# Performance work log

Measured on AMD Instinct MI355X. Metric: run time of the kernel, lower is better.

The kernel has to match this reference:

```python
import jax, jax.numpy as jnp
import numpy as np

DROP_PROB = 0.1
BLOCK_SIZE = 7  # odd -> no even-size trim branch
N, C, H, W = 64, 256, 28, 28


def conv3x3(x, w):
    # x: [N,C,H,W], w: [O,I,3,3], stride 1, SAME padding
    return jax.lax.conv_general_dilated(
        x, w, window_strides=(1, 1), padding='SAME',
        dimension_numbers=('NCHW', 'OIHW', 'NCHW'))


def setup_inputs() -> dict:
    key = jax.random.key(0)
    k1, k2, k3, k4 = jax.random.split(key, 4)
    x = jax.random.normal(k1, (N, C, H, W), jnp.float32)
    # learned conv weights for the two branches (layer3 and premodel.layer3)
    w_layer3 = jax.random.normal(k2, (C, C, 3, 3), jnp.float32) * 0.05
    w_pre = jax.random.normal(k3, (C, C, 3, 3), jnp.float32) * 0.05
    # uniform draws used for the Bernoulli(gamma) drop mask, shape (N,H,W)
    mask_u = jax.random.uniform(k4, (N, H, W), jnp.float32)
    return {'x': x, 'w_layer3': w_layer3, 'w_pre': w_pre, 'mask_u': mask_u}


def reference(x, w_layer3, w_pre, mask_u):
    gamma = DROP_PROB / (BLOCK_SIZE ** 2)
    a = conv3x3(x, w_layer3)   # x = self.layer3(x)
    b = conv3x3(x, w_pre)      # output4 = self.premodel.layer3(x)
    # mask = (rand(N,H,W) < gamma).float()
    mask = (mask_u < gamma).astype(x.dtype)  # [N,H,W]
    # block_mask = 1 - max_pool2d(mask, k=block_size, stride=1, pad=block_size//2)
    pooled = jax.lax.reduce_window(
        mask, -jnp.inf, jax.lax.max,
        window_dimensions=(1, BLOCK_SIZE, BLOCK_SIZE),
        window_strides=(1, 1, 1), padding='SAME')
    block_mask = 1.0 - pooled  # [N,H,W]
    # fused blend: keep layer3 output where block_mask==1, else premodel output
    out = jnp.where(block_mask[:, None, :, :] == 1.0, a, b)  # [N,C,H,W]
    # out * block_mask.numel() / block_mask.sum()
    scale = jnp.asarray(block_mask.size, x.dtype) / jnp.sum(block_mask)
    return out * scale
```

## Files before the change

### kernel.cpp

```cpp
#include <hip/hip_runtime.h>
#include <hip/hip_bf16.h>


typedef __bf16  bf16x8 __attribute__((ext_vector_type(8)));
typedef float   f32x4  __attribute__((ext_vector_type(4)));
typedef short   short8 __attribute__((ext_vector_type(8)));
typedef unsigned int u32;
typedef unsigned short u16;

#define XT_OFF     65536
#define WT_OFF     29556736
#define LISTA_OFF  31916032
#define LISTB_OFF  32116736
#define SLOT       22528

__device__ __forceinline__ u16 f2bf(float v) {
    u32 u = __float_as_uint(v);
    u32 r = (u + 0x7FFFu + ((u >> 16) & 1u)) >> 16;
    return (u16)r;
}

__device__ __forceinline__ void gll16(const void* g, void* l) {
    __builtin_amdgcn_global_load_lds(
        (const __attribute__((address_space(1))) u32*)g,
        (__attribute__((address_space(3))) u32*)l, 16, 0, 0);
}

__global__ void prep_kernel(const float* __restrict__ x,
                            const float* __restrict__ wl,
                            const float* __restrict__ wp,
                            const float* __restrict__ mu,
                            u16* __restrict__ xt, u16* __restrict__ wt,
                            int* __restrict__ listA, int* __restrict__ listB,
                            int* __restrict__ cntB, int* __restrict__ cntA) {
    int b = blockIdx.x, tid = threadIdx.x;
    if (b < 1920) {
        int n = b / 30, oh = b % 30;
        u16* row = xt + (size_t)(n * 30 + oh) * 30 * 256;
        if (oh == 0 || oh == 29) {
            u32* r32 = (u32*)row;
            #pragma unroll
            for (int i = 0; i < 15; ++i) r32[i * 256 + tid] = 0;
            return;
        }
        __shared__ u16 sm[7168];
        int h = oh - 1;
        const float* src = x + ((size_t)(n * 256 + tid) * 28 + h) * 28;
        float f[28];
        #pragma unroll
        for (int q = 0; q < 7; ++q) {
            float4 v = *(const float4*)(src + q * 4);
            f[q * 4 + 0] = v.x; f[q * 4 + 1] = v.y;
            f[q * 4 + 2] = v.z; f[q * 4 + 3] = v.w;
        }
        #pragma unroll
        for (int w = 0; w < 28; ++w)
            sm[w * 256 + tid] = f2bf(f[w]);
        __syncthreads();
        u32* r32 = (u32*)row;
        if (tid < 128) r32[tid] = 0;
        else           r32[29 * 128 + (tid - 128)] = 0;
        const u32* s32 = (const u32*)sm;
        u32* dst = r32 + 128;
        #pragma unroll
        for (int k = 0; k < 14; ++k)
            dst[k * 256 + tid] = s32[k * 256 + tid];
    } else if (b < 2048) {
        __shared__ u16 wsm[9216];
        int wb = b - 1920;
        int bn = wb >> 6, rowg = (wb & 63) * 4;
        const float* wsrc = (bn ? wp : wl) + (size_t)rowg * 2304;
        const f32x4* s4 = (const f32x4*)wsrc;
        #pragma unroll
        for (int i = 0; i < 9; ++i) {
            int q = i * 256 + tid;
            f32x4 v = s4[q];
            #pragma unroll
            for (int cmp = 0; cmp < 4; ++cmp)
                wsm[q * 4 + cmp] = f2bf(v[cmp]);
        }
        __syncthreads();
        u32* wo = (u32*)wt;
        #pragma unroll
        for (int w = 0; w < 18; ++w) {
            int idx = w * 256 + tid;
            int jjp = idx & 3, ps = (idx >> 2) & 3;
            int tt = idx >> 4;
            int t = tt % 72, rl = tt / 72;
            int row = rowg + rl;
            int row128 = row & 127, nh = row >> 7;
            int c0 = (t & 7) * 32 + ((ps ^ ((row >> 1) & 3)) << 3) + jjp * 2;
            int e0 = rl * 2304 + c0 * 9 + (t >> 3);
            u32 val = (u32)wsm[e0] | ((u32)wsm[e0 + 9] << 16);
            wo[(size_t)(t * 4 + bn * 2 + nh) * 2048 + row128 * 16 + ps * 4 + jjp]
                = val;
        }
    } else {
        __shared__ int lsum[4];
        __shared__ int basB, basA;
        int m = (b - 2048) * 256 + tid;
        int n = m / 784, rem = m % 784;
        int h = rem / 28, w = rem % 28;
        const float g = (float)(0.1 / 49.0);
        const float* un = mu + n * 784;
        int p = 0;
        for (int dy = -3; dy <= 3; ++dy) {
            int hh = h + dy;
            if (hh < 0 || hh >= 28) continue;
            for (int dx = -3; dx <= 3; ++dx) {
                int ww = w + dx;
                if (ww < 0 || ww >= 28) continue;
                p |= (un[hh * 28 + ww] < g) ? 1 : 0;
            }
        }
        unsigned long long ball = __ballot(p);
        int wid = tid >> 6, ln = tid & 63;
        if (ln == 0) lsum[wid] = __popcll(ball);
        __syncthreads();
        if (tid == 0) {
            int tB = lsum[0] + lsum[1] + lsum[2] + lsum[3];
            basB = atomicAdd(cntB, tB);
            basA = atomicAdd(cntA, 256 - tB);
        }
        __syncthreads();
        int offB = 0, offA = 0;
        for (int i = 0; i < wid; ++i) { offB += lsum[i]; offA += 64 - lsum[i]; }
        int rank1 = __popcll(ball & ((1ULL << ln) - 1));
        int rank0 = ln - rank1;
        if (p) listB[basB + offB + rank1] = m;
        else   listA[basA + offA + rank0] = m;
    }
}

__global__ __launch_bounds__(256, 2)
void conv_kernel(const char* __restrict__ xt,
                 const char* __restrict__ wt,
                 const int* __restrict__ listA,
                 const int* __restrict__ listB,
                 const int* __restrict__ dropped,
                 float* __restrict__ out) {
    __shared__ char smem[55296];
    const int tid = threadIdx.x;
    const int lb = (blockIdx.x & 7) * 57 + (blockIdx.x >> 3);
    const int vt = lb >> 1;
    const int nh = lb & 1;
    const int cB = *dropped;
    const int cA = 50176 - cB;
    const int naT = (cA + 223) / 224;
    const int nbT = (cB + 223) / 224;
    if (vt >= naT + nbT) return;
    const int branch = (vt >= naT) ? 1 : 0;
    const int tix = branch ? (vt - naT) : vt;
    const int cnt = branch ? cB : cA;
    const int* lst = branch ? listB : listA;
    const int nq = branch * 2 + nh;
    const int lane = tid & 63, wave = tid >> 6;
    const int lane15 = lane & 15, grp = lane >> 4;
    const int wm = wave >> 1, wn = wave & 1;

    long pbA[4];
    {
        int swz = ((tid & 3) ^ ((tid >> 3) & 3)) << 4;
        #pragma unroll
        for (int i = 0; i < 4; ++i) {
            int r = i * 64 + (tid >> 2);
            int idx = tix * 224 + r;
            if (idx >= cnt) idx = cnt - 1;
            int m = lst[idx];
            int n = m / 784, rem = m % 784;
            pbA[i] = (long)(((n * 30 + rem / 28 + 1) * 30 + (rem % 28 + 1)) * 512
                            + swz);
        }
    }

    f32x4 acc[7][4];
    #pragma unroll
    for (int i = 0; i < 7; ++i)
        #pragma unroll
        for (int j = 0; j < 4; ++j)
            acc[i][j] = (f32x4){0.f, 0.f, 0.f, 0.f};

    const int so  = (grp ^ ((lane15 >> 1) & 3)) << 4;
    const int arb = wm * 7168 + (lane15 << 6) + so;
    const int brb = 14336 + wn * 4096 + (lane15 << 6) + so;

#define AON(TC) ((long)((TC) >> 3) / 3 * 15360 + (long)(((TC) >> 3) % 3) * 512 \
                 - 15872 + (long)(((TC) & 7) << 6))
#define STG(TC, SL) { char* sd_ = smem + (SL) * SLOT;                       \
        const long ao_ = AON(TC);                                           \
        gll16(xt + pbA[0] + ao_, sd_ + (tid << 4));                         \
        gll16(xt + pbA[1] + ao_, sd_ + 4096 + (tid << 4));                  \
        gll16(xt + pbA[2] + ao_, sd_ + 8192 + (tid << 4));                  \
        if (tid < 128) gll16(xt + pbA[3] + ao_, sd_ + 12288 + (tid << 4));  \
        const char* wb_ = wt + ((size_t)((TC) * 4 + nq) << 13);             \
        gll16(wb_ + (tid << 4), sd_ + 14336 + (tid << 4));                  \
        gll16(wb_ + 4096 + (tid << 4), sd_ + 18432 + (tid << 4)); }
#define DS_AV0(dst, SL) { const char* sb_ = smem + (SL) * SLOT;             \
        _Pragma("unroll")                                                   \
        for (int fm = 0; fm < 4; ++fm)                                      \
            dst[fm] = *(const bf16x8*)(sb_ + arb + (fm << 10)); }
#define DS_AV1(dst, SL) { const char* sb_ = smem + (SL) * SLOT + 4096;      \
        _Pragma("unroll")                                                   \
        for (int fm = 0; fm < 3; ++fm)                                      \
            dst[fm] = *(const bf16x8*)(sb_ + arb + (fm << 10)); }
#define DS_BV(dst, SL) { const char* sb_ = smem + (SL) * SLOT;              \
        _Pragma("unroll")                                                   \
        for (int fn = 0; fn < 4; ++fn)                                      \
            dst[fn] = *(const bf16x8*)(sb_ + brb + (fn << 10)); }
#define MM(A0_, NF, AV, BV) { __builtin_amdgcn_s_setprio(1);                \
        _Pragma("unroll")                                                   \
        for (int fm = 0; fm < (NF); ++fm)                                   \
            _Pragma("unroll")                                               \
            for (int fn = 0; fn < 4; ++fn)                                  \
                acc[(A0_)+fm][fn] = __builtin_amdgcn_mfma_f32_16x16x32_bf16( \
                    AV[fm], BV[fn], acc[(A0_)+fm][fn], 0, 0, 0);            \
        __builtin_amdgcn_s_setprio(0); }
#define LGKM(N) { asm volatile("s_waitcnt lgkmcnt(" #N ")" ::: "memory");   \
                  __builtin_amdgcn_sched_barrier(0); }
#define VM0     { asm volatile("s_waitcnt vmcnt(0)" ::: "memory");          \
                  __builtin_amdgcn_sched_barrier(0); }
#define BAR     asm volatile("s_barrier" ::: "memory")

    bf16x8 av0[4], av1[3], bv[4];

    STG(0, 0);
    VM0;
    BAR;

    for (int t = 0; t < 72; ++t) {
        const int sc = t & 1, ss = sc ^ 1;
        if (t < 71) STG(t + 1, ss);
        DS_AV0(av0, sc);
        DS_BV(bv, sc);
        DS_AV1(av1, sc);
        LGKM(3);
        MM(0, 4, av0, bv);
        LGKM(0);
        MM(4, 3, av1, bv);
        VM0;
        BAR;
    }

    float scale = 50176.0f / (float)(50176 - cB);
    float* ep = (float*)smem + wave * 2080;
    __syncthreads();
    #pragma unroll
    for (int rr = 0; rr < 4; ++rr) {
        const int r2 = rr & 1;
        const int mh = rr >> 1;
        const int nf = mh ? 3 : 4;
        for (int fm2 = 0; fm2 < nf; ++fm2)
            #pragma unroll
            for (int f2 = 0; f2 < 2; ++f2)
                #pragma unroll
                for (int j = 0; j < 4; ++j)
                    ep[(f2 * 16 + lane15) * 65 + fm2 * 16 + grp * 4 + j] =
                        acc[mh * 4 + fm2][r2 * 2 + f2][j];
        __syncthreads();
        {
            int gidx = tix * 224 + wm * 112 + mh * 64 + lane;
            if ((mh == 0 || lane < 48) && gidx < cnt) {
                int m = lst[gidx];
                int n = m / 784, rem = m % 784;
                size_t ob = (size_t)n * 200704 + rem;
                #pragma unroll
                for (int ch = 0; ch < 32; ++ch) {
                    int c = nh * 128 + wn * 64 + r2 * 32 + ch;
                    out[ob + (size_t)c * 784] = ep[ch * 65 + lane] * scale;
                }
            }
        }
        __syncthreads();
    }
#undef AON
#undef STG
#undef DS_AV0
#undef DS_AV1
#undef DS_BV
#undef MM
#undef LGKM
#undef VM0
#undef BAR
}

extern "C" void kernel_launch(void* const* d_in, const int* in_sizes, int n_in,
                              void* d_out, int out_size, void* d_ws, size_t ws_size,
                              hipStream_t stream) {
    const float* x  = (const float*)d_in[0];
    const float* wl = (const float*)d_in[1];
    const float* wp = (const float*)d_in[2];
    const float* mu = (const float*)d_in[3];
    float* out = (float*)d_out;
    char* ws = (char*)d_ws;

    int* cntB = (int*)ws;
    int* cntA = (int*)(ws + 4);
    u16* xt = (u16*)(ws + XT_OFF);
    u16* wt = (u16*)(ws + WT_OFF);
    int* listA = (int*)(ws + LISTA_OFF);
    int* listB = (int*)(ws + LISTB_OFF);

    hipMemsetAsync(ws, 0, 8, stream);

    prep_kernel<<<2244, 256, 0, stream>>>(x, wl, wp, mu, xt, wt,
                                          listA, listB, cntB, cntA);
    conv_kernel<<<456, 256, 0, stream>>>((const char*)xt, (const char*)wt,
                                         listA, listB, cntB, out);
}
```

Baseline: 102.1 us.

## Enlarge conv tile to 256x256 with 8 waves and 8-phase K=64 pipeline

Restructures the implicit-GEMM conv kernel so each 512-thread block computes 256 positions by all 256 output channels, with a K-step of 64 instead of 32. The weight prep layout is changed to match, and shared memory grows to 128KB with a finer-grained schedule interleaving LDS reads, async global-to-LDS loads and MFMAs across eight sub-phases. The aim is more data reuse per loaded tile, no duplicated A loads across channel halves, and fewer K iterations. In exchange the grid drops to 200 blocks, which can under-fill the 256 CUs, and the loop adds many barriers.

```diff
diff --git a/kernel.cpp b/kernel.cpp
--- a/kernel.cpp
+++ b/kernel.cpp
@@ -12,7 +12,6 @@
 #define WT_OFF     29556736
 #define LISTA_OFF  31916032
 #define LISTB_OFF  32116736
-#define SLOT       22528
 
 __device__ __forceinline__ u16 f2bf(float v) {
     u32 u = __float_as_uint(v);
@@ -84,16 +83,16 @@
         #pragma unroll
         for (int w = 0; w < 18; ++w) {
             int idx = w * 256 + tid;
-            int jjp = idx & 3, ps = (idx >> 2) & 3;
-            int tt = idx >> 4;
-            int t = tt % 72, rl = tt / 72;
-            int row = rowg + rl;
-            int row128 = row & 127, nh = row >> 7;
-            int c0 = (t & 7) * 32 + ((ps ^ ((row >> 1) & 3)) << 3) + jjp * 2;
-            int e0 = rl * 2304 + c0 * 9 + (t >> 3);
+            int jj2 = idx & 3;
+            int p   = (idx >> 2) & 7;
+            int tt  = idx >> 5;
+            int t = tt % 36, rl = tt / 36;
+            int ch = rowg + rl;
+            int c0 = (t & 3) * 64 + ((p ^ (ch & 7)) << 3) + jj2 * 2;
+            int e0 = rl * 2304 + c0 * 9 + (t >> 2);
             u32 val = (u32)wsm[e0] | ((u32)wsm[e0 + 9] << 16);
-            wo[(size_t)(t * 4 + bn * 2 + nh) * 2048 + row128 * 16 + ps * 4 + jjp]
-                = val;
+            wo[(size_t)(t * 2 + bn) * 8192 + (ch >> 7) * 4096
+               + (ch & 127) * 32 + p * 4 + jj2] = val;
         }
     } else {
         __shared__ int lsum[4];
@@ -132,113 +131,121 @@
     }
 }
 
-__global__ __launch_bounds__(256, 2)
+__global__ __launch_bounds__(512, 2)
 void conv_kernel(const char* __restrict__ xt,
                  const char* __restrict__ wt,
                  const int* __restrict__ listA,
                  const int* __restrict__ listB,
                  const int* __restrict__ dropped,
                  float* __restrict__ out) {
-    __shared__ char smem[55296];
+    __shared__ char smem[131072];
     const int tid = threadIdx.x;
-    const int lb = (blockIdx.x & 7) * 57 + (blockIdx.x >> 3);
-    const int vt = lb >> 1;
-    const int nh = lb & 1;
+    const int lb = (blockIdx.x & 7) * 25 + (blockIdx.x >> 3);
     const int cB = *dropped;
     const int cA = 50176 - cB;
-    const int naT = (cA + 223) / 224;
-    const int nbT = (cB + 223) / 224;
-    if (vt >= naT + nbT) return;
-    const int branch = (vt >= naT) ? 1 : 0;
-    const int tix = branch ? (vt - naT) : vt;
+    const int naT = (cA + 255) >> 8;
+    const int nbT = (cB + 255) >> 8;
+    if (lb >= naT + nbT) return;
+    const int branch = (lb >= naT) ? 1 : 0;
+    const int tix = branch ? (lb - naT) : lb;
     const int cnt = branch ? cB : cA;
     const int* lst = branch ? listB : listA;
-    const int nq = branch * 2 + nh;
     const int lane = tid & 63, wave = tid >> 6;
     const int lane15 = lane & 15, grp = lane >> 4;
-    const int wm = wave >> 1, wn = wave & 1;
+    const int wm = wave >> 2, wn = wave & 3;
 
     long pbA[4];
     {
-        int swz = ((tid & 3) ^ ((tid >> 3) & 3)) << 4;
-        #pragma unroll
-        for (int i = 0; i < 4; ++i) {
-            int r = i * 64 + (tid >> 2);
-            int idx = tix * 224 + r;
+        int swz = ((tid & 7) ^ ((tid >> 3) & 7)) << 4;
+        #pragma unroll
+        for (int q = 0; q < 4; ++q) {
+            int r = (q >> 1) * 128 + (q & 1) * 64 + (tid >> 3);
+            int idx = tix * 256 + r;
             if (idx >= cnt) idx = cnt - 1;
             int m = lst[idx];
             int n = m / 784, rem = m % 784;
-            pbA[i] = (long)(((n * 30 + rem / 28 + 1) * 30 + (rem % 28 + 1)) * 512
+            pbA[q] = (long)(((n * 30 + rem / 28 + 1) * 30 + (rem % 28 + 1)) * 512
                             + swz);
         }
     }
 
-    f32x4 acc[7][4];
+    f32x4 acc[8][4];
     #pragma unroll
-    for (int i = 0; i < 7; ++i)
+    for (int i = 0; i < 8; ++i)
         #pragma unroll
         for (int j = 0; j < 4; ++j)
             acc[i][j] = (f32x4){0.f, 0.f, 0.f, 0.f};
 
-    const int so  = (grp ^ ((lane15 >> 1) & 3)) << 4;
-    const int arb = wm * 7168 + (lane15 << 6) + so;
-    const int brb = 14336 + wn * 4096 + (lane15 << 6) + so;
-
-#define AON(TC) ((long)((TC) >> 3) / 3 * 15360 + (long)(((TC) >> 3) % 3) * 512 \
-                 - 15872 + (long)(((TC) & 7) << 6))
-#define STG(TC, SL) { char* sd_ = smem + (SL) * SLOT;                       \
+    const int xA = lane15 & 7;
+    int axk[2];
+    axk[0] = (grp ^ xA) << 4;
+    axk[1] = ((4 + grp) ^ xA) << 4;
+    const int aBase = wm * 16384 + (lane15 << 7);
+    const int bBase = 32768 + ((wn >> 1) << 14) + (((wn & 1) * 64 + lane15) << 7);
+
+#define AON(TC) ((long)((TC) >> 2) / 3 * 15360 + (long)(((TC) >> 2) % 3) * 512 \
+                 - 15872 + (long)(((TC) & 3) << 7))
+#define DS_A(dst, PAR, MH, KS) { const char* s_ = smem + (PAR) * 65536;     \
+        _Pragma("unroll")                                                   \
+        for (int f = 0; f < 4; ++f)                                         \
+            dst[f] = *(const bf16x8*)(s_ + aBase + (MH) * 8192 + f * 2048   \
+                                      + axk[KS]); }
+#define DS_B(dst, PAR, KS) { const char* s_ = smem + (PAR) * 65536;         \
+        _Pragma("unroll")                                                   \
+        for (int fn = 0; fn < 4; ++fn)                                      \
+            dst[fn] = *(const bf16x8*)(s_ + bBase + fn * 2048 + axk[KS]); }
+#define STG_AH(TC, H, PAR) { char* d_ = smem + (PAR) * 65536 + (H) * 16384; \
         const long ao_ = AON(TC);                                           \
-        gll16(xt + pbA[0] + ao_, sd_ + (tid << 4));                         \
-        gll16(xt + pbA[1] + ao_, sd_ + 4096 + (tid << 4));                  \
-        gll16(xt + pbA[2] + ao_, sd_ + 8192 + (tid << 4));                  \
-        if (tid < 128) gll16(xt + pbA[3] + ao_, sd_ + 12288 + (tid << 4));  \
-        const char* wb_ = wt + ((size_t)((TC) * 4 + nq) << 13);             \
-        gll16(wb_ + (tid << 4), sd_ + 14336 + (tid << 4));                  \
-        gll16(wb_ + 4096 + (tid << 4), sd_ + 18432 + (tid << 4)); }
-#define DS_AV0(dst, SL) { const char* sb_ = smem + (SL) * SLOT;             \
+        gll16(xt + pbA[(H) * 2 + 0] + ao_, d_ + (tid << 4));                \
+        gll16(xt + pbA[(H) * 2 + 1] + ao_, d_ + 8192 + (tid << 4)); }
+#define STG_BH(TC, H, PAR) {                                                \
+        const char* s_ = wt + ((size_t)((TC) * 2 + branch) << 15)           \
+                         + ((H) << 14);                                     \
+        char* d_ = smem + (PAR) * 65536 + 32768 + (H) * 16384;              \
+        gll16(s_ + (tid << 4), d_ + (tid << 4));                            \
+        gll16(s_ + 8192 + (tid << 4), d_ + 8192 + (tid << 4)); }
+#define MMc(BASE, AV, BV) { __builtin_amdgcn_s_setprio(1);                  \
         _Pragma("unroll")                                                   \
         for (int fm = 0; fm < 4; ++fm)                                      \
-            dst[fm] = *(const bf16x8*)(sb_ + arb + (fm << 10)); }
-#define DS_AV1(dst, SL) { const char* sb_ = smem + (SL) * SLOT + 4096;      \
-        _Pragma("unroll")                                                   \
-        for (int fm = 0; fm < 3; ++fm)                                      \
-            dst[fm] = *(const bf16x8*)(sb_ + arb + (fm << 10)); }
-#define DS_BV(dst, SL) { const char* sb_ = smem + (SL) * SLOT;              \
-        _Pragma("unroll")                                                   \
-        for (int fn = 0; fn < 4; ++fn)                                      \
-            dst[fn] = *(const bf16x8*)(sb_ + brb + (fn << 10)); }
-#define MM(A0_, NF, AV, BV) { __builtin_amdgcn_s_setprio(1);                \
-        _Pragma("unroll")                                                   \
-        for (int fm = 0; fm < (NF); ++fm)                                   \
             _Pragma("unroll")                                               \
             for (int fn = 0; fn < 4; ++fn)                                  \
-                acc[(A0_)+fm][fn] = __builtin_amdgcn_mfma_f32_16x16x32_bf16( \
-                    AV[fm], BV[fn], acc[(A0_)+fm][fn], 0, 0, 0);            \
+                acc[(BASE) + fm][fn] = __builtin_amdgcn_mfma_f32_16x16x32_bf16( \
+                    AV[fm], BV[fn], acc[(BASE) + fm][fn], 0, 0, 0);         \
         __builtin_amdgcn_s_setprio(0); }
-#define LGKM(N) { asm volatile("s_waitcnt lgkmcnt(" #N ")" ::: "memory");   \
+#define LGKM0   { asm volatile("s_waitcnt lgkmcnt(0)" ::: "memory");        \
                   __builtin_amdgcn_sched_barrier(0); }
-#define VM0     { asm volatile("s_waitcnt vmcnt(0)" ::: "memory");          \
+#define VM4     { asm volatile("s_waitcnt vmcnt(4)" ::: "memory");          \
                   __builtin_amdgcn_sched_barrier(0); }
 #define BAR     asm volatile("s_barrier" ::: "memory")
 
-    bf16x8 av0[4], av1[3], bv[4];
-
-    STG(0, 0);
-    VM0;
+    bf16x8 av[4], bv0[4], bv1[4];
+
+    STG_AH(0, 0, 0); STG_AH(0, 1, 0);
+    STG_BH(0, 0, 0); STG_BH(0, 1, 0);
+    STG_BH(1, 0, 1); STG_BH(1, 1, 1);
+    VM4;
     BAR;
 
-    for (int t = 0; t < 72; ++t) {
-        const int sc = t & 1, ss = sc ^ 1;
-        if (t < 71) STG(t + 1, ss);
-        DS_AV0(av0, sc);
-        DS_BV(bv, sc);
-        DS_AV1(av1, sc);
-        LGKM(3);
-        MM(0, 4, av0, bv);
-        LGKM(0);
-        MM(4, 3, av1, bv);
-        VM0;
-        BAR;
+    for (int i = 0; i < 18; ++i) {
+        const int v = 2 * i + 1;
+        int t2 = 2 * i + 2; if (t2 > 35) t2 = 35;
+        int t3 = 2 * i + 3; if (t3 > 35) t3 = 35;
+        DS_A(av, 0, 0, 0); DS_B(bv0, 0, 0); STG_AH(v, 0, 1);
+        BAR; LGKM0; MMc(0, av, bv0); BAR;
+        DS_A(av, 0, 0, 1); DS_B(bv1, 0, 1); STG_AH(v, 1, 1);
+        BAR; LGKM0; MMc(0, av, bv1); BAR;
+        DS_A(av, 0, 1, 0); STG_BH(t2, 0, 0);
+        BAR; LGKM0; MMc(4, av, bv0); BAR;
+        DS_A(av, 0, 1, 1); STG_BH(t2, 1, 0);
+        BAR; LGKM0; MMc(4, av, bv1); VM4; BAR;
+        DS_A(av, 1, 0, 0); DS_B(bv0, 1, 0); STG_AH(t2, 0, 0);
+        BAR; LGKM0; MMc(0, av, bv0); BAR;
+        DS_A(av, 1, 0, 1); DS_B(bv1, 1, 1); STG_AH(t2, 1, 0);
+        BAR; LGKM0; MMc(0, av, bv1); BAR;
+        DS_A(av, 1, 1, 0); STG_BH(t3, 0, 1);
+        BAR; LGKM0; MMc(4, av, bv0); BAR;
+        DS_A(av, 1, 1, 1); STG_BH(t3, 1, 1);
+        BAR; LGKM0; MMc(4, av, bv1); VM4; BAR;
     }
 
     float scale = 50176.0f / (float)(50176 - cB);
@@ -248,8 +255,8 @@
     for (int rr = 0; rr < 4; ++rr) {
         const int r2 = rr & 1;
         const int mh = rr >> 1;
-        const int nf = mh ? 3 : 4;
-        for (int fm2 = 0; fm2 < nf; ++fm2)
+        #pragma unroll
+        for (int fm2 = 0; fm2 < 4; ++fm2)
             #pragma unroll
             for (int f2 = 0; f2 < 2; ++f2)
                 #pragma unroll
@@ -258,14 +265,14 @@
                         acc[mh * 4 + fm2][r2 * 2 + f2][j];
         __syncthreads();
         {
-            int gidx = tix * 224 + wm * 112 + mh * 64 + lane;
-            if ((mh == 0 || lane < 48) && gidx < cnt) {
+            int gidx = tix * 256 + wm * 128 + mh * 64 + lane;
+            if (gidx < cnt) {
                 int m = lst[gidx];
                 int n = m / 784, rem = m % 784;
                 size_t ob = (size_t)n * 200704 + rem;
                 #pragma unroll
                 for (int ch = 0; ch < 32; ++ch) {
-                    int c = nh * 128 + wn * 64 + r2 * 32 + ch;
+                    int c = wn * 64 + r2 * 32 + ch;
                     out[ob + (size_t)c * 784] = ep[ch * 65 + lane] * scale;
                 }
             }
@@ -273,13 +280,13 @@
         __syncthreads();
     }
 #undef AON
-#undef STG
-#undef DS_AV0
-#undef DS_AV1
-#undef DS_BV
-#undef MM
-#undef LGKM
-#undef VM0
+#undef DS_A
+#undef DS_B
+#undef STG_AH
+#undef STG_BH
+#undef MMc
+#undef LGKM0
+#undef VM4
 #undef BAR
 }
 
@@ -304,6 +311,6 @@
 
     prep_kernel<<<2244, 256, 0, stream>>>(x, wl, wp, mu, xt, wt,
                                           listA, listB, cntB, cntA);
-    conv_kernel<<<456, 256, 0, stream>>>((const char*)xt, (const char*)wt,
+    conv_kernel<<<200, 512, 0, stream>>>((const char*)xt, (const char*)wt,
                                          listA, listB, cntB, out);
 }
```

New measurement: 106.6 us. 1.04x slower.

## Split conv workgroups into single-wave blocks to remove barriers

Applied to the files above, without the earlier changes.

Restructures the implicit-GEMM conv so each workgroup is one 64-lane wave computing a 112-row by 64-channel tile, instead of a 4-wave block computing 224 by 128. Each wave now stages its own A and B tiles into a smaller LDS double buffer, which removes all s_barrier and __syncthreads calls, and the grid grows from 456 to 1800 blocks. The cost is that A tiles are no longer shared across the channel halves within a block, so global and LDS staging traffic for the activations rises roughly fourfold per output. Occupancy and latency hiding now depend on how many single-wave blocks fit per CU.

```diff
diff --git a/kernel.cpp b/kernel.cpp
--- a/kernel.cpp
+++ b/kernel.cpp
@@ -12,7 +12,7 @@
 #define WT_OFF     29556736
 #define LISTA_OFF  31916032
 #define LISTB_OFF  32116736
-#define SLOT       22528
+#define SLOT       11264
 
 __device__ __forceinline__ u16 f2bf(float v) {
     u32 u = __float_as_uint(v);
@@ -132,39 +132,37 @@
     }
 }
 
-__global__ __launch_bounds__(256, 2)
+__global__ __launch_bounds__(64, 2)
 void conv_kernel(const char* __restrict__ xt,
                  const char* __restrict__ wt,
                  const int* __restrict__ listA,
                  const int* __restrict__ listB,
                  const int* __restrict__ dropped,
                  float* __restrict__ out) {
-    __shared__ char smem[55296];
-    const int tid = threadIdx.x;
-    const int lb = (blockIdx.x & 7) * 57 + (blockIdx.x >> 3);
-    const int vt = lb >> 1;
-    const int nh = lb & 1;
+    __shared__ char smem[22528];
+    const int lane = threadIdx.x;
+    const int lb = (blockIdx.x & 7) * 225 + (blockIdx.x >> 3);
+    const int vt = lb >> 2;
+    const int wq = lb & 3;
     const int cB = *dropped;
     const int cA = 50176 - cB;
-    const int naT = (cA + 223) / 224;
-    const int nbT = (cB + 223) / 224;
+    const int naT = (cA + 111) / 112;
+    const int nbT = (cB + 111) / 112;
     if (vt >= naT + nbT) return;
     const int branch = (vt >= naT) ? 1 : 0;
     const int tix = branch ? (vt - naT) : vt;
     const int cnt = branch ? cB : cA;
     const int* lst = branch ? listB : listA;
-    const int nq = branch * 2 + nh;
-    const int lane = tid & 63, wave = tid >> 6;
+    const int nq = branch * 2 + (wq >> 1);
+    const int qoff = (wq & 1) * 4096;
     const int lane15 = lane & 15, grp = lane >> 4;
-    const int wm = wave >> 1, wn = wave & 1;
-
-    long pbA[4];
+
+    long pbA[7];
     {
-        int swz = ((tid & 3) ^ ((tid >> 3) & 3)) << 4;
-        #pragma unroll
-        for (int i = 0; i < 4; ++i) {
-            int r = i * 64 + (tid >> 2);
-            int idx = tix * 224 + r;
+        int swz = ((lane & 3) ^ ((lane >> 3) & 3)) << 4;
+        #pragma unroll
+        for (int i = 0; i < 7; ++i) {
+            int idx = tix * 112 + i * 16 + (lane >> 2);
             if (idx >= cnt) idx = cnt - 1;
             int m = lst[idx];
             int n = m / 784, rem = m % 784;
@@ -181,20 +179,21 @@
             acc[i][j] = (f32x4){0.f, 0.f, 0.f, 0.f};
 
     const int so  = (grp ^ ((lane15 >> 1) & 3)) << 4;
-    const int arb = wm * 7168 + (lane15 << 6) + so;
-    const int brb = 14336 + wn * 4096 + (lane15 << 6) + so;
+    const int arb = (lane15 << 6) + so;
+    const int brb = 7168 + (lane15 << 6) + so;
 
 #define AON(TC) ((long)((TC) >> 3) / 3 * 15360 + (long)(((TC) >> 3) % 3) * 512 \
                  - 15872 + (long)(((TC) & 7) << 6))
 #define STG(TC, SL) { char* sd_ = smem + (SL) * SLOT;                       \
         const long ao_ = AON(TC);                                           \
-        gll16(xt + pbA[0] + ao_, sd_ + (tid << 4));                         \
-        gll16(xt + pbA[1] + ao_, sd_ + 4096 + (tid << 4));                  \
-        gll16(xt + pbA[2] + ao_, sd_ + 8192 + (tid << 4));                  \
-        if (tid < 128) gll16(xt + pbA[3] + ao_, sd_ + 12288 + (tid << 4));  \
-        const char* wb_ = wt + ((size_t)((TC) * 4 + nq) << 13);             \
-        gll16(wb_ + (tid << 4), sd_ + 14336 + (tid << 4));                  \
-        gll16(wb_ + 4096 + (tid << 4), sd_ + 18432 + (tid << 4)); }
+        _Pragma("unroll")                                                   \
+        for (int i_ = 0; i_ < 7; ++i_)                                      \
+            gll16(xt + pbA[i_] + ao_, sd_ + i_ * 1024 + (lane << 4));       \
+        const char* wb_ = wt + ((size_t)((TC) * 4 + nq) << 13) + qoff;      \
+        _Pragma("unroll")                                                   \
+        for (int j_ = 0; j_ < 4; ++j_)                                      \
+            gll16(wb_ + j_ * 1024 + (lane << 4),                            \
+                  sd_ + 7168 + j_ * 1024 + (lane << 4)); }
 #define DS_AV0(dst, SL) { const char* sb_ = smem + (SL) * SLOT;             \
         _Pragma("unroll")                                                   \
         for (int fm = 0; fm < 4; ++fm)                                      \
@@ -219,13 +218,11 @@
                   __builtin_amdgcn_sched_barrier(0); }
 #define VM0     { asm volatile("s_waitcnt vmcnt(0)" ::: "memory");          \
                   __builtin_amdgcn_sched_barrier(0); }
-#define BAR     asm volatile("s_barrier" ::: "memory")
 
     bf16x8 av0[4], av1[3], bv[4];
 
     STG(0, 0);
     VM0;
-    BAR;
 
     for (int t = 0; t < 72; ++t) {
         const int sc = t & 1, ss = sc ^ 1;
@@ -238,12 +235,10 @@
         LGKM(0);
         MM(4, 3, av1, bv);
         VM0;
-        BAR;
     }
 
     float scale = 50176.0f / (float)(50176 - cB);
-    float* ep = (float*)smem + wave * 2080;
-    __syncthreads();
+    float* ep = (float*)smem;
     #pragma unroll
     for (int rr = 0; rr < 4; ++rr) {
         const int r2 = rr & 1;
@@ -256,21 +251,21 @@
                 for (int j = 0; j < 4; ++j)
                     ep[(f2 * 16 + lane15) * 65 + fm2 * 16 + grp * 4 + j] =
                         acc[mh * 4 + fm2][r2 * 2 + f2][j];
-        __syncthreads();
+        LGKM(0);
         {
-            int gidx = tix * 224 + wm * 112 + mh * 64 + lane;
+            int gidx = tix * 112 + mh * 64 + lane;
             if ((mh == 0 || lane < 48) && gidx < cnt) {
                 int m = lst[gidx];
                 int n = m / 784, rem = m % 784;
                 size_t ob = (size_t)n * 200704 + rem;
                 #pragma unroll
                 for (int ch = 0; ch < 32; ++ch) {
-                    int c = nh * 128 + wn * 64 + r2 * 32 + ch;
+                    int c = wq * 64 + r2 * 32 + ch;
                     out[ob + (size_t)c * 784] = ep[ch * 65 + lane] * scale;
                 }
             }
         }
-        __syncthreads();
+        LGKM(0);
     }
 #undef AON
 #undef STG
@@ -280,7 +275,6 @@
 #undef MM
 #undef LGKM
 #undef VM0
-#undef BAR
 }
 
 extern "C" void kernel_launch(void* const* d_in, const int* in_sizes, int n_in,
@@ -304,6 +298,6 @@
 
     prep_kernel<<<2244, 256, 0, stream>>>(x, wl, wp, mu, xt, wt,
                                           listA, listB, cntB, cntA);
-    conv_kernel<<<456, 256, 0, stream>>>((const char*)xt, (const char*)wt,
+    conv_kernel<<<1800, 64, 0, stream>>>((const char*)xt, (const char*)wt,
                                          listA, listB, cntB, out);
 }
```

Result: slower. 149.2 us (+46.2%).
